# Kernel optimization log

Hardware: AMD Instinct MI355X
Metric: run time of the kernel (lower is better)

## Reference

```python
import jax, jax.numpy as jnp
import numpy as np

B, T, D, H = 64, 512, 1024, 1024


def setup_inputs() -> dict:
    key = jax.random.key(0)
    ks = jax.random.split(key, 9)
    s = 1.0 / np.sqrt(H)
    return {
        "x": jax.random.normal(ks[0], (B, T, D), dtype=jnp.float32),
        "w_ih": jax.random.uniform(ks[1], (4 * H, D), jnp.float32, -s, s),
        "w_hh": jax.random.uniform(ks[2], (4 * H, H), jnp.float32, -s, s),
        "b_ih": jax.random.uniform(ks[3], (4 * H,), jnp.float32, -s, s),
        "b_hh": jax.random.uniform(ks[4], (4 * H,), jnp.float32, -s, s),
        "w_gender": jax.random.normal(ks[5], (2, H), dtype=jnp.float32) * s,
        "b_gender": jnp.zeros((2,), jnp.float32),
        "w_age": jax.random.normal(ks[6], (7, H), dtype=jnp.float32) * s,
        "b_age": jnp.zeros((7,), jnp.float32),
    }


def _lstm_final_h(x, w_ih, w_hh, b_ih, b_hh):
    # x: [B, T, D]; torch LSTM gate order (i, f, g, o), both biases added.
    b, t, _ = x.shape
    h = w_hh.shape[1]
    # Precompute input contribution for all timesteps in one GEMM: [T, B, 4H]
    xg = jnp.swapaxes(jnp.einsum("btd,gd->btg", x, w_ih) + (b_ih + b_hh), 0, 1)

    def step(carry, xt):
        hprev, cprev = carry
        gates = xt + hprev @ w_hh.T  # [B, 4H]
        i, f, g, o = jnp.split(gates, 4, axis=-1)
        i = jax.nn.sigmoid(i)
        f = jax.nn.sigmoid(f)
        g = jnp.tanh(g)
        o = jax.nn.sigmoid(o)
        c = f * cprev + i * g
        hnew = o * jnp.tanh(c)
        return (hnew, c), None

    z = jnp.zeros((b, h), x.dtype)
    (h_final, _), _ = jax.lax.scan(step, (z, z), xg)
    return h_final  # [B, H]


def reference(x, w_ih, w_hh, b_ih, b_hh, w_gender, b_gender, w_age, b_age):
    h = _lstm_final_h(x, w_ih, w_hh, b_ih, b_hh)
    gender = h @ w_gender.T + b_gender  # [B, 2]
    age = h @ w_age.T + b_age          # [B, 7]
    return (gender, age)
```

## Files before the change

kernel.cpp:

```cpp
#include <hip/hip_runtime.h>
#include <stdint.h>

#define WB 64
#define WT 512
#define WD 1024
#define WH 1024
#define G4H 4096

typedef __bf16 bf16x8 __attribute__((ext_vector_type(8)));
typedef float f32x4 __attribute__((ext_vector_type(4)));
typedef unsigned long long u64;
#define MFMA16(a, b, c) __builtin_amdgcn_mfma_f32_16x16x32_bf16((a), (b), (c), 0, 0, 0)

__device__ __forceinline__ unsigned short f2bf(float f) {
  union { float f; unsigned u; } v; v.f = f;
  unsigned r = v.u + 0x7FFFu + ((v.u >> 16) & 1u);
  return (unsigned short)(r >> 16);
}
__device__ __forceinline__ float bf2f(unsigned short h) {
  union { unsigned u; float f; } v; v.u = ((unsigned)h) << 16;
  return v.f;
}
__device__ __forceinline__ float sig_(float x) { return 1.0f / (1.0f + __expf(-x)); }
__device__ __forceinline__ float tanh_(float x) { return 2.0f / (1.0f + __expf(-2.0f * x)) - 1.0f; }

__global__ void k_init(unsigned* __restrict__ flags, uint4* __restrict__ h0) {
  int t = threadIdx.x;
  if (t < 256) flags[t] = 0u;
  for (int i = t; i < (WB * WH * 2 / 16); i += 256) h0[i] = make_uint4(0, 0, 0, 0);
}

__global__ void k_cvt(const float* __restrict__ src, unsigned short* __restrict__ dst, int n8) {
  int i = blockIdx.x * 256 + threadIdx.x;
  if (i >= n8) return;
  const float4* s = (const float4*)src + (size_t)i * 2;
  float4 a = s[0], b = s[1];
  union { unsigned short us[8]; uint4 v; } o;
  o.us[0] = f2bf(a.x); o.us[1] = f2bf(a.y); o.us[2] = f2bf(a.z); o.us[3] = f2bf(a.w);
  o.us[4] = f2bf(b.x); o.us[5] = f2bf(b.y); o.us[6] = f2bf(b.z); o.us[7] = f2bf(b.w);
  ((uint4*)dst)[i] = o.v;
}

__global__ void k_prep_whh(const float* __restrict__ whh, unsigned short* __restrict__ dst) {
  int idx = blockIdx.x * 256 + threadIdx.x;
  int n = idx & 63, kb = (idx >> 6) & 127, jb = idx >> 13;
  int gate = n & 3;
  int jl = ((n >> 4) << 2) | ((n >> 2) & 3);
  int row = gate * WH + jb * 16 + jl;
  const float4* s = (const float4*)(whh + (size_t)row * WH + kb * 8);
  float4 a = s[0], b = s[1];
  union { unsigned short us[8]; uint4 v; } o;
  o.us[0] = f2bf(a.x); o.us[1] = f2bf(a.y); o.us[2] = f2bf(a.z); o.us[3] = f2bf(a.w);
  o.us[4] = f2bf(b.x); o.us[5] = f2bf(b.y); o.us[6] = f2bf(b.z); o.us[7] = f2bf(b.w);
  *(uint4*)(dst + (size_t)idx * 8) = o.v;
}

__global__ void k_xg_gemm(const unsigned short* __restrict__ xb,
                          const unsigned short* __restrict__ wihb,
                          const float* __restrict__ bih, const float* __restrict__ bhh,
                          float* __restrict__ xg,
                          int t0, int lTc) {
  __shared__ __align__(16) unsigned short As[4 * 128 * 8];
  __shared__ __align__(16) unsigned short Bs[4 * 128 * 8];
  const int tid = threadIdx.x;
  const int bm = blockIdx.x, bn = blockIdx.y;
  const int w = tid >> 6, lane = tid & 63, quad = lane >> 4, l15 = lane & 15;
  const int wm = (w >> 1) * 64, wn = (w & 1) * 64;
  const int TcM = (1 << lTc) - 1;
  f32x4 acc[4][4];
#pragma unroll
  for (int i = 0; i < 4; ++i)
#pragma unroll
    for (int j = 0; j < 4; ++j) acc[i][j] = 0.f;

  for (int kt = 0; kt < 32; ++kt) {
    const int k0 = kt * 32;
    __syncthreads();
#pragma unroll
    for (int rr = 0; rr < 2; ++rr) {
      int s = rr * 256 + tid;
      int kb = s >> 7, m = s & 127;
      int mg = bm * 128 + m;
      int b = mg >> lTc, tt = mg & TcM;
      size_t xrow = (size_t)b * WT + t0 + tt;
      *(uint4*)(As + (size_t)s * 8) = *(const uint4*)(xb + xrow * WD + k0 + kb * 8);
      size_t wrow = (size_t)(bn * 128 + m);
      *(uint4*)(Bs + (size_t)s * 8) = *(const uint4*)(wihb + wrow * WD + k0 + kb * 8);
    }
    __syncthreads();
    bf16x8 af[4], bfv[4];
#pragma unroll
    for (int mt = 0; mt < 4; ++mt)
      af[mt] = *(const bf16x8*)(As + ((size_t)(quad * 128 + wm + mt * 16 + l15)) * 8);
#pragma unroll
    for (int nt = 0; nt < 4; ++nt)
      bfv[nt] = *(const bf16x8*)(Bs + ((size_t)(quad * 128 + wn + nt * 16 + l15)) * 8);
#pragma unroll
    for (int mt = 0; mt < 4; ++mt)
#pragma unroll
      for (int nt = 0; nt < 4; ++nt) acc[mt][nt] = MFMA16(af[mt], bfv[nt], acc[mt][nt]);
  }
#pragma unroll
  for (int nt = 0; nt < 4; ++nt) {
    int n = bn * 128 + wn + nt * 16 + l15;
    float bias = bih[n] + bhh[n];
#pragma unroll
    for (int mt = 0; mt < 4; ++mt) {
#pragma unroll
      for (int r = 0; r < 4; ++r) {
        int mg = bm * 128 + wm + mt * 16 + quad * 4 + r;
        int b = mg >> lTc, tt = mg & TcM;
        xg[((size_t)tt * WB + b) * G4H + n] = acc[mt][nt][r] + bias;
      }
    }
  }
}

__global__ void __launch_bounds__(256, 1)
k_lstm(const unsigned short* __restrict__ wprep,
       const float* __restrict__ xg,
       unsigned short* __restrict__ hbuf,
       float* __restrict__ cbuf,
       unsigned* __restrict__ flags,
       int t0, int Tc) {
  __shared__ __align__(16) unsigned short hA[128 * 16 * 8];
  __shared__ __align__(8) unsigned short hOut[16][16];
  const int tid = threadIdx.x;
  const int wg = blockIdx.x;
  const int bg = wg >> 6;
  const int jb = wg & 63;
  const int w = tid >> 6;
  const int lane = tid & 63;
  const int quad = lane >> 4;
  const int l15 = lane & 15;
  const int gate = l15 & 3;
  const int jl = (w << 2) | (l15 >> 2);
  const int jglob = jb * 16 + jl;

  bf16x8 bfr[32];
  {
    const bf16x8* wp = (const bf16x8*)wprep + (size_t)jb * (128 * 64);
#pragma unroll
    for (int kk = 0; kk < 32; ++kk)
      bfr[kk] = wp[(kk * 4 + quad) * 64 + (w * 16 + l15)];
  }

  float c[4];
  if (t0 == 0) {
    c[0] = c[1] = c[2] = c[3] = 0.f;
  } else {
#pragma unroll
    for (int r = 0; r < 4; ++r)
      c[r] = cbuf[(size_t)(bg * 16 + quad * 4 + r) * WH + jglob];
  }

  for (int t = t0; t < t0 + Tc; ++t) {
    const float* xgt = xg + (size_t)(t - t0) * (WB * G4H);
    const int row = gate * WH + jglob;
    float xgv[4];
#pragma unroll
    for (int r = 0; r < 4; ++r)
      xgv[r] = xgt[(size_t)(bg * 16 + quad * 4 + r) * G4H + row];

    if (w == 0) {
      const unsigned target = (unsigned)t;
      int guard = 0;
      while (true) {
        unsigned v = __hip_atomic_load(&flags[bg * 64 + lane], __ATOMIC_RELAXED,
                                       __HIP_MEMORY_SCOPE_AGENT);
        if (__ballot(v >= target) == ~0ull) break;
        __builtin_amdgcn_s_sleep(2);
        if (++guard > (1 << 22)) break;
      }
    }
    __syncthreads();

    {
      const u64* hsrc8 = (const u64*)(hbuf + (size_t)(t & 1) * (WB * WH));
#pragma unroll
      for (int r = 0; r < 8; ++r) {
        int s = r * 256 + tid;
        int kb = s >> 4, m = s & 15;
        size_t base8 = (size_t)(bg * 16 + m) * 256 + (size_t)kb * 2;
        u64 lo = __hip_atomic_load(hsrc8 + base8, __ATOMIC_RELAXED, __HIP_MEMORY_SCOPE_AGENT);
        u64 hi = __hip_atomic_load(hsrc8 + base8 + 1, __ATOMIC_RELAXED, __HIP_MEMORY_SCOPE_AGENT);
        union { u64 q[2]; uint4 v; } u;
        u.q[0] = lo; u.q[1] = hi;
        *(uint4*)(hA + (size_t)s * 8) = u.v;
      }
    }
    __syncthreads();

    f32x4 acc[4];
    acc[0] = 0.f; acc[1] = 0.f; acc[2] = 0.f; acc[3] = 0.f;
#pragma unroll
    for (int kk = 0; kk < 32; ++kk) {
      bf16x8 a = *(const bf16x8*)(hA + ((size_t)((kk * 4 + quad) * 16 + l15)) * 8);
      acc[kk & 3] = MFMA16(a, bfr[kk], acc[kk & 3]);
    }
    f32x4 d = acc[0] + acc[1] + acc[2] + acc[3];
    float act[4];
#pragma unroll
    for (int r = 0; r < 4; ++r) {
      float pre = d[r] + xgv[r];
      act[r] = (gate == 2) ? tanh_(pre) : sig_(pre);
    }
    float hnew[4];
#pragma unroll
    for (int r = 0; r < 4; ++r) {
      int base = lane & ~3;
      float iv = __shfl(act[r], base + 0, 64);
      float fv = __shfl(act[r], base + 1, 64);
      float gv = __shfl(act[r], base + 2, 64);
      float ov = __shfl(act[r], base + 3, 64);
      c[r] = fv * c[r] + iv * gv;
      hnew[r] = ov * tanh_(c[r]);
    }
    if (gate == 0) {
#pragma unroll
      for (int r = 0; r < 4; ++r) hOut[quad * 4 + r][jl] = f2bf(hnew[r]);
    }
    __syncthreads();
    if (tid < 64) {
      int m = tid >> 2, c4 = (tid & 3) << 2;
      u64 v = *(const u64*)&hOut[m][c4];
      u64* dst = (u64*)(hbuf + (size_t)((t + 1) & 1) * (WB * WH)
                        + (size_t)(bg * 16 + m) * WH + jb * 16 + c4);
      __hip_atomic_store(dst, v, __ATOMIC_RELAXED, __HIP_MEMORY_SCOPE_AGENT);
    }
    __syncthreads();
    if (tid == 0)
      __hip_atomic_store(&flags[wg], (unsigned)(t + 1), __ATOMIC_RELAXED,
                         __HIP_MEMORY_SCOPE_AGENT);
  }
  if (gate == 0) {
#pragma unroll
    for (int r = 0; r < 4; ++r)
      cbuf[(size_t)(bg * 16 + quad * 4 + r) * WH + jglob] = c[r];
  }
}

__global__ void k_heads(const unsigned short* __restrict__ h,
                        const float* __restrict__ wgd, const float* __restrict__ bgd,
                        const float* __restrict__ wag, const float* __restrict__ bag,
                        float* __restrict__ out) {
  int b = blockIdx.x;
  int lane = threadIdx.x;
  float acc[9];
#pragma unroll
  for (int o = 0; o < 9; ++o) acc[o] = 0.f;
  for (int k = lane; k < WH; k += 64) {
    float hk = bf2f(h[(size_t)b * WH + k]);
#pragma unroll
    for (int o = 0; o < 2; ++o) acc[o] += hk * wgd[o * WH + k];
#pragma unroll
    for (int o = 0; o < 7; ++o) acc[2 + o] += hk * wag[o * WH + k];
  }
#pragma unroll
  for (int o = 0; o < 9; ++o)
    for (int s = 32; s; s >>= 1) acc[o] += __shfl_xor(acc[o], s, 64);
  if (lane == 0) {
    out[b * 2 + 0] = acc[0] + bgd[0];
    out[b * 2 + 1] = acc[1] + bgd[1];
#pragma unroll
    for (int o = 0; o < 7; ++o) out[WB * 2 + b * 7 + o] = acc[2 + o] + bag[o];
  }
}

extern "C" void kernel_launch(void* const* d_in, const int* in_sizes, int n_in,
                              void* d_out, int out_size, void* d_ws, size_t ws_size,
                              hipStream_t stream) {
  const float* x = (const float*)d_in[0];
  const float* w_ih = (const float*)d_in[1];
  const float* w_hh = (const float*)d_in[2];
  const float* b_ih = (const float*)d_in[3];
  const float* b_hh = (const float*)d_in[4];
  const float* w_gender = (const float*)d_in[5];
  const float* b_gender = (const float*)d_in[6];
  const float* w_age = (const float*)d_in[7];
  const float* b_age = (const float*)d_in[8];
  float* out = (float*)d_out;

  char* ws = (char*)d_ws;
  size_t off = 0;
  auto alloc = [&](size_t bytes) -> void* {
    void* p = ws + off;
    off = (off + bytes + 255) & ~(size_t)255;
    return p;
  };
  unsigned* flags = (unsigned*)alloc(256 * sizeof(unsigned));
  unsigned short* hbuf = (unsigned short*)alloc((size_t)2 * WB * WH * 2);
  float* cbuf = (float*)alloc((size_t)WB * WH * 4);
  unsigned short* xb = (unsigned short*)alloc((size_t)WB * WT * WD * 2);
  unsigned short* wihb = (unsigned short*)alloc((size_t)G4H * WD * 2);
  unsigned short* whhp = (unsigned short*)alloc((size_t)G4H * WD * 2);
  size_t fixed = off;
  int lTc = 7;
  while (lTc > 1 && fixed + (((size_t)1 << lTc) * WB * G4H * 4) > ws_size) --lTc;
  int Tc = 1 << lTc;
  float* xg = (float*)alloc((size_t)Tc * WB * G4H * 4);

  k_init<<<1, 256, 0, stream>>>(flags, (uint4*)hbuf);
  k_cvt<<<(WB * WT * WD / 8 + 255) / 256, 256, 0, stream>>>(x, xb, WB * WT * WD / 8);
  k_cvt<<<(G4H * WD / 8 + 255) / 256, 256, 0, stream>>>(w_ih, wihb, G4H * WD / 8);
  k_prep_whh<<<G4H * WD / (8 * 256), 256, 0, stream>>>(w_hh, whhp);

  for (int t0 = 0; t0 < WT; t0 += Tc) {
    dim3 g(WB * Tc / 128, G4H / 128);
    k_xg_gemm<<<g, 256, 0, stream>>>(xb, wihb, b_ih, b_hh, xg, t0, lTc);
    const unsigned short* wp = whhp;
    const float* xgp = xg;
    unsigned short* hp = hbuf;
    float* cp = cbuf;
    unsigned* fl = flags;
    int t0v = t0, Tcv = Tc;
    void* args[] = {(void*)&wp, (void*)&xgp, (void*)&hp, (void*)&cp, (void*)&fl,
                    (void*)&t0v, (void*)&Tcv};
    hipLaunchCooperativeKernel((const void*)k_lstm, dim3(256), dim3(256), args, 0, stream);
  }
  k_heads<<<WB, 64, 0, stream>>>(hbuf, w_gender, b_gender, w_age, b_age, out);
}
```

Baseline: 3.834 ms.

## Load h directly into MFMA registers and drop per-step barriers in LSTM recurrence

Every wave now polls the neighbour flags itself, so the barrier after the spin-wait is gone. The LDS staging of h is also gone: each wave reads its A fragments straight from global memory with relaxed atomic loads, double-buffered in groups of eight and interleaved with the MFMAs. The flag publish step waits on the vmcnt counter within wave 0 instead of taking a second block barrier. This trims synchronisation and LDS round-trips on the serial critical path, at the cost of four waves issuing redundant global loads and polling. It also depends on relaxed ordering plus waitcnt for correctness of the h publication.

Result: slower. 6.503 ms (+69.6%).

```diff
diff --git a/kernel.cpp b/kernel.cpp
--- a/kernel.cpp
+++ b/kernel.cpp
@@ -23,6 +23,12 @@
 }
 __device__ __forceinline__ float sig_(float x) { return 1.0f / (1.0f + __expf(-x)); }
 __device__ __forceinline__ float tanh_(float x) { return 2.0f / (1.0f + __expf(-2.0f * x)) - 1.0f; }
+__device__ __forceinline__ bf16x8 mk8(u64 lo, u64 hi) {
+  union { u64 q[2]; bf16x8 v; } u; u.q[0] = lo; u.q[1] = hi; return u.v;
+}
+__device__ __forceinline__ u64 aload8(const u64* p) {
+  return __hip_atomic_load(p, __ATOMIC_RELAXED, __HIP_MEMORY_SCOPE_AGENT);
+}
 
 __global__ void k_init(unsigned* __restrict__ flags, uint4* __restrict__ h0) {
   int t = threadIdx.x;
@@ -123,7 +129,6 @@
        float* __restrict__ cbuf,
        unsigned* __restrict__ flags,
        int t0, int Tc) {
-  __shared__ __align__(16) unsigned short hA[128 * 16 * 8];
   __shared__ __align__(8) unsigned short hOut[16][16];
   const int tid = threadIdx.x;
   const int wg = blockIdx.x;
@@ -154,51 +159,56 @@
       c[r] = cbuf[(size_t)(bg * 16 + quad * 4 + r) * WH + jglob];
   }
 
+  const int row = gate * WH + jglob;
+
   for (int t = t0; t < t0 + Tc; ++t) {
     const float* xgt = xg + (size_t)(t - t0) * (WB * G4H);
-    const int row = gate * WH + jglob;
     float xgv[4];
 #pragma unroll
     for (int r = 0; r < 4; ++r)
       xgv[r] = xgt[(size_t)(bg * 16 + quad * 4 + r) * G4H + row];
 
-    if (w == 0) {
+    {
       const unsigned target = (unsigned)t;
       int guard = 0;
       while (true) {
         unsigned v = __hip_atomic_load(&flags[bg * 64 + lane], __ATOMIC_RELAXED,
                                        __HIP_MEMORY_SCOPE_AGENT);
         if (__ballot(v >= target) == ~0ull) break;
-        __builtin_amdgcn_s_sleep(2);
+        __builtin_amdgcn_s_sleep(1);
         if (++guard > (1 << 22)) break;
       }
     }
-    __syncthreads();
-
-    {
-      const u64* hsrc8 = (const u64*)(hbuf + (size_t)(t & 1) * (WB * WH));
-#pragma unroll
-      for (int r = 0; r < 8; ++r) {
-        int s = r * 256 + tid;
-        int kb = s >> 4, m = s & 15;
-        size_t base8 = (size_t)(bg * 16 + m) * 256 + (size_t)kb * 2;
-        u64 lo = __hip_atomic_load(hsrc8 + base8, __ATOMIC_RELAXED, __HIP_MEMORY_SCOPE_AGENT);
-        u64 hi = __hip_atomic_load(hsrc8 + base8 + 1, __ATOMIC_RELAXED, __HIP_MEMORY_SCOPE_AGENT);
-        union { u64 q[2]; uint4 v; } u;
-        u.q[0] = lo; u.q[1] = hi;
-        *(uint4*)(hA + (size_t)s * 8) = u.v;
-      }
-    }
-    __syncthreads();
-
+    __atomic_signal_fence(__ATOMIC_SEQ_CST);
+
+    const u64* h8 = (const u64*)(hbuf + (size_t)(t & 1) * (WB * WH))
+                    + (size_t)(bg * 16 + l15) * 256 + quad * 2;
     f32x4 acc[4];
     acc[0] = 0.f; acc[1] = 0.f; acc[2] = 0.f; acc[3] = 0.f;
-#pragma unroll
-    for (int kk = 0; kk < 32; ++kk) {
-      bf16x8 a = *(const bf16x8*)(hA + ((size_t)((kk * 4 + quad) * 16 + l15)) * 8);
-      acc[kk & 3] = MFMA16(a, bfr[kk], acc[kk & 3]);
+    u64 qlo[2][8], qhi[2][8];
+#pragma unroll
+    for (int j = 0; j < 8; ++j) {
+      qlo[0][j] = aload8(h8 + (size_t)j * 8);
+      qhi[0][j] = aload8(h8 + (size_t)j * 8 + 1);
+    }
+#pragma unroll
+    for (int g = 0; g < 4; ++g) {
+      if (g < 3) {
+#pragma unroll
+        for (int j = 0; j < 8; ++j) {
+          int kk = (g + 1) * 8 + j;
+          qlo[(g + 1) & 1][j] = aload8(h8 + (size_t)kk * 8);
+          qhi[(g + 1) & 1][j] = aload8(h8 + (size_t)kk * 8 + 1);
+        }
+      }
+#pragma unroll
+      for (int j = 0; j < 8; ++j) {
+        int kk = g * 8 + j;
+        acc[kk & 3] = MFMA16(mk8(qlo[g & 1][j], qhi[g & 1][j]), bfr[kk], acc[kk & 3]);
+      }
     }
     f32x4 d = acc[0] + acc[1] + acc[2] + acc[3];
+
     float act[4];
 #pragma unroll
     for (int r = 0; r < 4; ++r) {
@@ -221,17 +231,19 @@
       for (int r = 0; r < 4; ++r) hOut[quad * 4 + r][jl] = f2bf(hnew[r]);
     }
     __syncthreads();
-    if (tid < 64) {
-      int m = tid >> 2, c4 = (tid & 3) << 2;
+    if (w == 0) {
+      int m = lane >> 2, c4 = (lane & 3) << 2;
       u64 v = *(const u64*)&hOut[m][c4];
       u64* dst = (u64*)(hbuf + (size_t)((t + 1) & 1) * (WB * WH)
                         + (size_t)(bg * 16 + m) * WH + jb * 16 + c4);
       __hip_atomic_store(dst, v, __ATOMIC_RELAXED, __HIP_MEMORY_SCOPE_AGENT);
-    }
-    __syncthreads();
-    if (tid == 0)
-      __hip_atomic_store(&flags[wg], (unsigned)(t + 1), __ATOMIC_RELAXED,
-                         __HIP_MEMORY_SCOPE_AGENT);
+      __atomic_signal_fence(__ATOMIC_SEQ_CST);
+      __builtin_amdgcn_s_waitcnt(0x0f70);
+      __atomic_signal_fence(__ATOMIC_SEQ_CST);
+      if (lane == 0)
+        __hip_atomic_store(&flags[wg], (unsigned)(t + 1), __ATOMIC_RELAXED,
+                           __HIP_MEMORY_SCOPE_AGENT);
+    }
   }
   if (gate == 0) {
 #pragma unroll
```

## Overlap next chunk's input GEMM with LSTM recurrence in one cooperative launch

Applied to the files above, without the earlier changes.

Fuses the input-projection GEMM for the next time chunk into the cooperative LSTM kernel. Extra blocks (ids 256 and up) compute it into a double-buffered xg while the first 256 blocks run the recurrence on the current chunk. The chunk size drops to 64 and launch bounds allow two blocks per CU. The h write-back now packs values with shuffles and stores them directly, removing an LDS staging step and one barrier. The risk is that GEMM blocks sharing CUs with the latency-bound recurrence blocks slow each step through contention, and register pressure rises under the new launch bound.

New measurement: 4.343 ms. 1.13x slower.

```diff
diff --git a/kernel.cpp b/kernel.cpp
--- a/kernel.cpp
+++ b/kernel.cpp
@@ -23,6 +23,12 @@
 }
 __device__ __forceinline__ float sig_(float x) { return 1.0f / (1.0f + __expf(-x)); }
 __device__ __forceinline__ float tanh_(float x) { return 2.0f / (1.0f + __expf(-2.0f * x)) - 1.0f; }
+__device__ __forceinline__ u64 aload8(const u64* p) {
+  return __hip_atomic_load(p, __ATOMIC_RELAXED, __HIP_MEMORY_SCOPE_AGENT);
+}
+__device__ __forceinline__ void astore8(u64* p, u64 v) {
+  __hip_atomic_store(p, v, __ATOMIC_RELAXED, __HIP_MEMORY_SCOPE_AGENT);
+}
 
 __global__ void k_init(unsigned* __restrict__ flags, uint4* __restrict__ h0) {
   int t = threadIdx.x;
@@ -55,15 +61,11 @@
   *(uint4*)(dst + (size_t)idx * 8) = o.v;
 }
 
-__global__ void k_xg_gemm(const unsigned short* __restrict__ xb,
-                          const unsigned short* __restrict__ wihb,
-                          const float* __restrict__ bih, const float* __restrict__ bhh,
-                          float* __restrict__ xg,
-                          int t0, int lTc) {
-  __shared__ __align__(16) unsigned short As[4 * 128 * 8];
-  __shared__ __align__(16) unsigned short Bs[4 * 128 * 8];
-  const int tid = threadIdx.x;
-  const int bm = blockIdx.x, bn = blockIdx.y;
+__device__ __forceinline__ void gemm_tile(
+    unsigned short* As, unsigned short* Bs,
+    const unsigned short* __restrict__ xb, const unsigned short* __restrict__ wihb,
+    const float* __restrict__ bih, const float* __restrict__ bhh,
+    float* __restrict__ xg, int t0, int lTc, int bm, int bn, int tid) {
   const int w = tid >> 6, lane = tid & 63, quad = lane >> 4, l15 = lane & 15;
   const int wm = (w >> 1) * 64, wn = (w & 1) * 64;
   const int TcM = (1 << lTc) - 1;
@@ -116,17 +118,46 @@
   }
 }
 
-__global__ void __launch_bounds__(256, 1)
-k_lstm(const unsigned short* __restrict__ wprep,
-       const float* __restrict__ xg,
-       unsigned short* __restrict__ hbuf,
-       float* __restrict__ cbuf,
-       unsigned* __restrict__ flags,
-       int t0, int Tc) {
-  __shared__ __align__(16) unsigned short hA[128 * 16 * 8];
-  __shared__ __align__(8) unsigned short hOut[16][16];
+__global__ void k_xg_gemm(const unsigned short* __restrict__ xb,
+                          const unsigned short* __restrict__ wihb,
+                          const float* __restrict__ bih, const float* __restrict__ bhh,
+                          float* __restrict__ xg, int t0, int lTc) {
+  __shared__ __align__(16) unsigned short As[4 * 128 * 8];
+  __shared__ __align__(16) unsigned short Bs[4 * 128 * 8];
+  gemm_tile(As, Bs, xb, wihb, bih, bhh, xg, t0, lTc, blockIdx.x, blockIdx.y, threadIdx.x);
+}
+
+__global__ void __launch_bounds__(256, 2)
+k_fused(const unsigned short* __restrict__ wprep,
+        const float* __restrict__ xgr,
+        unsigned short* __restrict__ hbuf,
+        float* __restrict__ cbuf,
+        unsigned* __restrict__ flags,
+        int t0, int Tc,
+        const unsigned short* __restrict__ xb,
+        const unsigned short* __restrict__ wihb,
+        const float* __restrict__ bih, const float* __restrict__ bhh,
+        float* __restrict__ xgw,
+        int t0w, int lTc, int do_gemm) {
+  __shared__ __align__(16) unsigned char smem[32768];
+  const int bid = blockIdx.x;
   const int tid = threadIdx.x;
-  const int wg = blockIdx.x;
+
+  if (bid >= 256) {
+    if (!do_gemm) return;
+    unsigned short* As = (unsigned short*)smem;
+    unsigned short* Bs = (unsigned short*)(smem + 8192);
+    const int bmN = (WB << lTc) >> 7;
+    const int total = bmN * (G4H / 128);
+    for (int tile = bid - 256; tile < total; tile += 256) {
+      int bm = tile % bmN, bn = tile / bmN;
+      gemm_tile(As, Bs, xb, wihb, bih, bhh, xgw, t0w, lTc, bm, bn, tid);
+    }
+    return;
+  }
+
+  unsigned short* hA = (unsigned short*)smem;
+  const int wg = bid;
   const int bg = wg >> 6;
   const int jb = wg & 63;
   const int w = tid >> 6;
@@ -154,9 +185,10 @@
       c[r] = cbuf[(size_t)(bg * 16 + quad * 4 + r) * WH + jglob];
   }
 
+  const int row = gate * WH + jglob;
+
   for (int t = t0; t < t0 + Tc; ++t) {
-    const float* xgt = xg + (size_t)(t - t0) * (WB * G4H);
-    const int row = gate * WH + jglob;
+    const float* xgt = xgr + (size_t)(t - t0) * (WB * G4H);
     float xgv[4];
 #pragma unroll
     for (int r = 0; r < 4; ++r)
@@ -182,8 +214,8 @@
         int s = r * 256 + tid;
         int kb = s >> 4, m = s & 15;
         size_t base8 = (size_t)(bg * 16 + m) * 256 + (size_t)kb * 2;
-        u64 lo = __hip_atomic_load(hsrc8 + base8, __ATOMIC_RELAXED, __HIP_MEMORY_SCOPE_AGENT);
-        u64 hi = __hip_atomic_load(hsrc8 + base8 + 1, __ATOMIC_RELAXED, __HIP_MEMORY_SCOPE_AGENT);
+        u64 lo = aload8(hsrc8 + base8);
+        u64 hi = aload8(hsrc8 + base8 + 1);
         union { u64 q[2]; uint4 v; } u;
         u.q[0] = lo; u.q[1] = hi;
         *(uint4*)(hA + (size_t)s * 8) = u.v;
@@ -199,6 +231,7 @@
       acc[kk & 3] = MFMA16(a, bfr[kk], acc[kk & 3]);
     }
     f32x4 d = acc[0] + acc[1] + acc[2] + acc[3];
+
     float act[4];
 #pragma unroll
     for (int r = 0; r < 4; ++r) {
@@ -216,17 +249,18 @@
       c[r] = fv * c[r] + iv * gv;
       hnew[r] = ov * tanh_(c[r]);
     }
-    if (gate == 0) {
-#pragma unroll
-      for (int r = 0; r < 4; ++r) hOut[quad * 4 + r][jl] = f2bf(hnew[r]);
-    }
-    __syncthreads();
-    if (tid < 64) {
-      int m = tid >> 2, c4 = (tid & 3) << 2;
-      u64 v = *(const u64*)&hOut[m][c4];
-      u64* dst = (u64*)(hbuf + (size_t)((t + 1) & 1) * (WB * WH)
-                        + (size_t)(bg * 16 + m) * WH + jb * 16 + c4);
-      __hip_atomic_store(dst, v, __ATOMIC_RELAXED, __HIP_MEMORY_SCOPE_AGENT);
+
+    unsigned short* hdst = hbuf + (size_t)((t + 1) & 1) * (WB * WH);
+#pragma unroll
+    for (int r = 0; r < 4; ++r) {
+      union { unsigned short s[4]; u64 q; } pk;
+#pragma unroll
+      for (int p = 0; p < 4; ++p)
+        pk.s[p] = f2bf(__shfl(hnew[r], (lane & 48) + 4 * p, 64));
+      if (l15 == 0) {
+        u64* dst = (u64*)(hdst + (size_t)(bg * 16 + quad * 4 + r) * WH + jb * 16 + w * 4);
+        astore8(dst, pk.q);
+      }
     }
     __syncthreads();
     if (tid == 0)
@@ -295,28 +329,53 @@
   unsigned short* wihb = (unsigned short*)alloc((size_t)G4H * WD * 2);
   unsigned short* whhp = (unsigned short*)alloc((size_t)G4H * WD * 2);
   size_t fixed = off;
-  int lTc = 7;
-  while (lTc > 1 && fixed + (((size_t)1 << lTc) * WB * G4H * 4) > ws_size) --lTc;
+  int lTc = 6;
+  while (lTc > 1 && fixed + 2 * (((size_t)1 << lTc) * WB * G4H * 4) > ws_size) --lTc;
   int Tc = 1 << lTc;
-  float* xg = (float*)alloc((size_t)Tc * WB * G4H * 4);
+  float* xg0 = (float*)alloc((size_t)Tc * WB * G4H * 4);
+  float* xg1 = (float*)alloc((size_t)Tc * WB * G4H * 4);
+  float* xgb[2] = {xg0, xg1};
+  int nch = WT >> lTc;
+
+  int maxb = 0;
+  (void)hipOccupancyMaxActiveBlocksPerMultiprocessor(&maxb, k_fused, 256, 0);
+  const bool fused_ok = (maxb >= 2);
 
   k_init<<<1, 256, 0, stream>>>(flags, (uint4*)hbuf);
   k_cvt<<<(WB * WT * WD / 8 + 255) / 256, 256, 0, stream>>>(x, xb, WB * WT * WD / 8);
   k_cvt<<<(G4H * WD / 8 + 255) / 256, 256, 0, stream>>>(w_ih, wihb, G4H * WD / 8);
   k_prep_whh<<<G4H * WD / (8 * 256), 256, 0, stream>>>(w_hh, whhp);
 
-  for (int t0 = 0; t0 < WT; t0 += Tc) {
-    dim3 g(WB * Tc / 128, G4H / 128);
-    k_xg_gemm<<<g, 256, 0, stream>>>(xb, wihb, b_ih, b_hh, xg, t0, lTc);
+  dim3 gg((WB << lTc) / 128, G4H / 128);
+  k_xg_gemm<<<gg, 256, 0, stream>>>(xb, wihb, b_ih, b_hh, xgb[0], 0, lTc);
+
+  for (int k = 0; k < nch; ++k) {
     const unsigned short* wp = whhp;
-    const float* xgp = xg;
+    const float* xgr = xgb[k & 1];
     unsigned short* hp = hbuf;
     float* cp = cbuf;
     unsigned* fl = flags;
-    int t0v = t0, Tcv = Tc;
-    void* args[] = {(void*)&wp, (void*)&xgp, (void*)&hp, (void*)&cp, (void*)&fl,
-                    (void*)&t0v, (void*)&Tcv};
-    hipLaunchCooperativeKernel((const void*)k_lstm, dim3(256), dim3(256), args, 0, stream);
+    int t0v = k << lTc, Tcv = Tc;
+    const unsigned short* xbp = xb;
+    const unsigned short* wihp = wihb;
+    const float* bihp = b_ih;
+    const float* bhhp = b_hh;
+    float* xgw = xgb[(k + 1) & 1];
+    int t0w = (k + 1) << lTc;
+    int lTcv = lTc;
+    int dog = (fused_ok && (k + 1 < nch)) ? 1 : 0;
+    void* args[] = {(void*)&wp,   (void*)&xgr,  (void*)&hp,   (void*)&cp,
+                    (void*)&fl,   (void*)&t0v,  (void*)&Tcv,  (void*)&xbp,
+                    (void*)&wihp, (void*)&bihp, (void*)&bhhp, (void*)&xgw,
+                    (void*)&t0w,  (void*)&lTcv, (void*)&dog};
+    if (fused_ok) {
+      hipLaunchCooperativeKernel((const void*)k_fused, dim3(512), dim3(256), args, 0, stream);
+    } else {
+      hipLaunchCooperativeKernel((const void*)k_fused, dim3(256), dim3(256), args, 0, stream);
+      if (k + 1 < nch)
+        k_xg_gemm<<<gg, 256, 0, stream>>>(xb, wihb, b_ih, b_hh, xgb[(k + 1) & 1],
+                                          (k + 1) << lTc, lTc);
+    }
   }
   k_heads<<<WB, 64, 0, stream>>>(hbuf, w_gender, b_gender, w_age, b_age, out);
 }
```
